# Kernel optimization log

Hardware: AMD Instinct MI355X
Metric: run time of the kernel (lower is better)

Reference implementation:

```python
import jax, jax.numpy as jnp
import numpy as np

B, H, S, D = 4, 16, 2048, 64

def setup_inputs() -> dict:
    key = jax.random.key(0)
    kq, kk, kv = jax.random.split(key, 3)
    return {
        "query": jax.random.normal(kq, (B, H, S, D), dtype=jnp.float32),
        "key": jax.random.normal(kk, (B, H, S, D), dtype=jnp.float32),
        "value": jax.random.normal(kv, (B, H, S, D), dtype=jnp.float32),
        "dropout_p": 0,
    }

def reference(query, key, value, dropout_p):
    # qk: [B,H,S,S] materialized as in the original (unfused SDPA)
    scale = query.shape[-1] ** -0.5
    qk = jnp.einsum("bhqd,bhkd->bhqk", query, key) * scale
    attn = jax.nn.softmax(qk, axis=-1)
    # dropout_p == 0 -> identity (keeps reference deterministic)
    out = jnp.einsum("bhqk,bhkd->bhqd", attn, value)
    return out
```

## Files before the change

kernel.cpp:

```cpp
#include <hip/hip_runtime.h>
#include <hip/hip_bf16.h>

#define B_   4
#define H_   16
#define SEQ  2048
#define DH   64
#define BM   128
#define BN   64
#define NBH  (B_ * H_)
#define NELEM (NBH * SEQ * DH)

typedef __bf16 bf16x8 __attribute__((ext_vector_type(8)));
typedef float  f32x4  __attribute__((ext_vector_type(4)));
typedef unsigned short u16x8 __attribute__((ext_vector_type(8)));
typedef unsigned short u16x4 __attribute__((ext_vector_type(4)));

__device__ __forceinline__ unsigned short f2bu(float x) {
    __hip_bfloat16 h = __float2bfloat16(x);
    return __builtin_bit_cast(unsigned short, h);
}

__device__ __forceinline__ void ld_lds16(const unsigned short* g, unsigned short* l) {
    __builtin_amdgcn_global_load_lds(
        (const __attribute__((address_space(1))) unsigned int*)(g),
        (__attribute__((address_space(3))) unsigned int*)(l), 16, 0, 0);
}

__global__ __launch_bounds__(256)
void prep_kv(const float* __restrict__ K, const float* __restrict__ V,
             unsigned short* __restrict__ Kb, unsigned short* __restrict__ Vt) {
    __shared__ unsigned short tile[64 * 72];
    const int bh = blockIdx.y;
    const int s0 = blockIdx.x * 64;
    const int t  = threadIdx.x;

    {
        const float* Ki = K + (size_t)bh * SEQ * DH + (size_t)s0 * DH;
        unsigned short* Ko = Kb + (size_t)bh * SEQ * DH + (size_t)s0 * DH;
        for (int jj = 0; jj < 2; ++jj) {
            const int e = (jj * 256 + t) * 8;
            const float4 a = *reinterpret_cast<const float4*>(Ki + e);
            const float4 b = *reinterpret_cast<const float4*>(Ki + e + 4);
            u16x8 u;
            u[0] = f2bu(a.x); u[1] = f2bu(a.y); u[2] = f2bu(a.z); u[3] = f2bu(a.w);
            u[4] = f2bu(b.x); u[5] = f2bu(b.y); u[6] = f2bu(b.z); u[7] = f2bu(b.w);
            *reinterpret_cast<u16x8*>(Ko + e) = u;
        }
    }

    const float* Vb = V + (size_t)bh * SEQ * DH + (size_t)s0 * DH;
    unsigned short* Vo = Vt + (size_t)bh * DH * SEQ;
    {
        const int sl = t >> 2, d0 = (t & 3) * 16;
        for (int c = 0; c < 4; ++c) {
            const float4 v = *reinterpret_cast<const float4*>(Vb + sl * DH + d0 + c * 4);
            u16x4 u; u[0] = f2bu(v.x); u[1] = f2bu(v.y); u[2] = f2bu(v.z); u[3] = f2bu(v.w);
            *reinterpret_cast<u16x4*>(&tile[sl * 72 + d0 + c * 4]) = u;
        }
    }
    __syncthreads();
    {
        const int d = t >> 2, sc0 = (t & 3) * 16;
        for (int c = 0; c < 2; ++c) {
            const int s = sc0 + c * 8;
            u16x8 u;
#pragma unroll
            for (int r = 0; r < 8; ++r) u[r] = tile[(s + r) * 72 + d];
            *reinterpret_cast<u16x8*>(Vo + (size_t)d * SEQ + s0 + s) = u;
        }
    }
}

__global__ __launch_bounds__(256, 4)
void fa_fwd(const float* __restrict__ Qg, const unsigned short* __restrict__ Kb,
            const unsigned short* __restrict__ Vtb, float* __restrict__ Og)
{
    __shared__ __attribute__((aligned(16))) unsigned short smem[16384];

    const int tid  = threadIdx.x;
    const int lane = tid & 63;
    const int wave = tid >> 6;
    const int l15  = lane & 15;
    const int quad = lane >> 4;

    const int bid   = blockIdx.x;
    const int xcd   = bid & 7;
    const int jj    = bid >> 3;
    const int bh    = (xcd << 3) | (jj >> 4);
    const int qtile = jj & 15;

    const float*          Qb  = Qg  + (size_t)bh * SEQ * DH;
    const unsigned short* Kbh = Kb  + (size_t)bh * SEQ * DH;
    const unsigned short* Vbh = Vtb + (size_t)bh * DH * SEQ;
    float*                Ob  = Og  + (size_t)bh * SEQ * DH;

    const int qrow0 = qtile * BM + wave * 32;

    const float CS = 0.125f * 1.4426950408889634f;

    bf16x8 Qf[2][2];
    for (int rt = 0; rt < 2; ++rt) {
        const float* qsrc = Qb + (size_t)(qrow0 + rt * 16 + l15) * DH + quad * 8;
        for (int kt = 0; kt < 2; ++kt) {
            const float4 a = *reinterpret_cast<const float4*>(qsrc + kt * 32);
            const float4 b = *reinterpret_cast<const float4*>(qsrc + kt * 32 + 4);
            union { bf16x8 v; unsigned short u[8]; } tmp;
            tmp.u[0] = f2bu(a.x * CS); tmp.u[1] = f2bu(a.y * CS);
            tmp.u[2] = f2bu(a.z * CS); tmp.u[3] = f2bu(a.w * CS);
            tmp.u[4] = f2bu(b.x * CS); tmp.u[5] = f2bu(b.y * CS);
            tmp.u[6] = f2bu(b.z * CS); tmp.u[7] = f2bu(b.w * CS);
            Qf[rt][kt] = tmp.v;
        }
    }

    bf16x8 ones;
    {
        union { bf16x8 v; unsigned short u[8]; } t;
        for (int i = 0; i < 8; ++i) t.u[i] = 0x3F80;
        ones = t.v;
    }
    const f32x4 fzero = {0.f, 0.f, 0.f, 0.f};

    f32x4 Oacc[2][4];
    f32x4 Lacc[2];
    for (int rt = 0; rt < 2; ++rt) {
        Lacc[rt] = fzero;
        for (int dt = 0; dt < 4; ++dt) Oacc[rt][dt] = fzero;
    }

    const unsigned short* kp[2];
    const unsigned short* vp[2];
    int koff_st[2], voff_st[2];
    for (int i = 0; i < 2; ++i) {
        const int beta = i * 256 + tid;
        {
            const int s    = beta >> 3;
            const int b    = beta & 7;
            const int gnat = b ^ (s & 7);
            const int grow = 32 * ((s >> 4) & 1) + 8 * ((s >> 2) & 3)
                           + 4 * (s >> 5) + (s & 3);
            kp[i]  = Kbh + (size_t)grow * DH + gnat * 8;
        }
        {
            const int d = beta >> 3;
            const int g = (beta & 7) ^ (d & 7);
            vp[i]  = Vbh + (size_t)d * SEQ + g * 8;
        }
        koff_st[i] = (i * 256 + wave * 64) * 8;
        voff_st[i] = 4096 + (i * 256 + wave * 64) * 8;
    }

    int krd[4][2];
#pragma unroll
    for (int nt = 0; nt < 4; ++nt) {
        const int s  = nt * 16 + l15;
        const int sx = l15 & 7;
        krd[nt][0] = s * 64 + ((quad    ) ^ sx) * 8;
        krd[nt][1] = s * 64 + ((quad + 4) ^ sx) * 8;
    }
    int vrd[2][4];
#pragma unroll
    for (int ks = 0; ks < 2; ++ks)
#pragma unroll
        for (int dt = 0; dt < 4; ++dt) {
            const int d = dt * 16 + l15;
            vrd[ks][dt] = 4096 + d * 64 + (((ks * 4 + quad) ^ (l15 & 7)) << 3);
        }

#define STAGE(BUF) do {                                                        \
        _Pragma("unroll")                                                      \
        for (int i = 0; i < 2; ++i) {                                          \
            ld_lds16(kp[i], smem + (BUF) * 8192 + koff_st[i]);                 \
            kp[i] += BN * DH;                                                  \
        }                                                                      \
        _Pragma("unroll")                                                      \
        for (int i = 0; i < 2; ++i) {                                          \
            ld_lds16(vp[i], smem + (BUF) * 8192 + voff_st[i]);                 \
            vp[i] += BN;                                                       \
        }                                                                      \
    } while (0)

#define COMPUTE(BUF) do {                                                      \
        f32x4 Sacc[2][4];                                                      \
        __builtin_amdgcn_s_setprio(1);                                         \
        _Pragma("unroll")                                                      \
        for (int nt = 0; nt < 4; ++nt) {                                       \
            const bf16x8 kf0 = *reinterpret_cast<const bf16x8*>(               \
                &smem[(BUF) * 8192 + krd[nt][0]]);                             \
            const bf16x8 kf1 = *reinterpret_cast<const bf16x8*>(               \
                &smem[(BUF) * 8192 + krd[nt][1]]);                             \
            Sacc[0][nt] = __builtin_amdgcn_mfma_f32_16x16x32_bf16(kf0, Qf[0][0], fzero,       0, 0, 0); \
            Sacc[0][nt] = __builtin_amdgcn_mfma_f32_16x16x32_bf16(kf1, Qf[0][1], Sacc[0][nt], 0, 0, 0); \
            Sacc[1][nt] = __builtin_amdgcn_mfma_f32_16x16x32_bf16(kf0, Qf[1][0], fzero,       0, 0, 0); \
            Sacc[1][nt] = __builtin_amdgcn_mfma_f32_16x16x32_bf16(kf1, Qf[1][1], Sacc[1][nt], 0, 0, 0); \
        }                                                                      \
        __builtin_amdgcn_s_setprio(0);                                         \
        bf16x8 af[2][2];                                                       \
        _Pragma("unroll")                                                      \
        for (int rt = 0; rt < 2; ++rt)                                         \
        {                                                                      \
            _Pragma("unroll")                                                  \
            for (int ks = 0; ks < 2; ++ks) {                                   \
                union { bf16x8 v; unsigned w[4]; } a;                          \
                _Pragma("unroll")                                              \
                for (int h = 0; h < 2; ++h) {                                  \
                    _Pragma("unroll")                                          \
                    for (int rp = 0; rp < 2; ++rp) {                           \
                        const float p0 = __builtin_amdgcn_exp2f(Sacc[rt][ks + 2 * h][2 * rp    ]); \
                        const float p1 = __builtin_amdgcn_exp2f(Sacc[rt][ks + 2 * h][2 * rp + 1]); \
                        const unsigned u0 = __builtin_bit_cast(unsigned, p0) + 0x8000u; \
                        const unsigned u1 = __builtin_bit_cast(unsigned, p1) + 0x8000u; \
                        a.w[h * 2 + rp] = __builtin_amdgcn_perm(u1, u0, 0x07060302u); \
                    }                                                          \
                }                                                              \
                af[rt][ks] = a.v;                                              \
                Lacc[rt] = __builtin_amdgcn_mfma_f32_16x16x32_bf16(a.v, ones, Lacc[rt], 0, 0, 0); \
            }                                                                  \
        }                                                                      \
        __builtin_amdgcn_s_setprio(1);                                         \
        _Pragma("unroll")                                                      \
        for (int ks = 0; ks < 2; ++ks) {                                       \
            _Pragma("unroll")                                                  \
            for (int dt = 0; dt < 4; ++dt) {                                   \
                const bf16x8 bfr = *reinterpret_cast<const bf16x8*>(           \
                    &smem[(BUF) * 8192 + vrd[ks][dt]]);                        \
                Oacc[0][dt] = __builtin_amdgcn_mfma_f32_16x16x32_bf16(af[0][ks], bfr, Oacc[0][dt], 0, 0, 0); \
                Oacc[1][dt] = __builtin_amdgcn_mfma_f32_16x16x32_bf16(af[1][ks], bfr, Oacc[1][dt], 0, 0, 0); \
            }                                                                  \
        }                                                                      \
        __builtin_amdgcn_s_setprio(0);                                         \
    } while (0)

    STAGE(0);
    __syncthreads();

#pragma unroll 1
    for (int it2 = 0; it2 < 15; ++it2) {
        STAGE(1);
        COMPUTE(0);
        __syncthreads();
        STAGE(0);
        COMPUTE(1);
        __syncthreads();
    }
    STAGE(1);
    COMPUTE(0);
    __syncthreads();
    COMPUTE(1);

#undef STAGE
#undef COMPUTE

    for (int rt = 0; rt < 2; ++rt) {
        for (int r = 0; r < 4; ++r) {
            const float inv = 1.0f / Lacc[rt][r];
            const int row = qrow0 + rt * 16 + quad * 4 + r;
            float* orow = Ob + (size_t)row * DH + l15;
            for (int dt = 0; dt < 4; ++dt)
                orow[dt * 16] = Oacc[rt][dt][r] * inv;
        }
    }
}

extern "C" void kernel_launch(void* const* d_in, const int* in_sizes, int n_in,
                              void* d_out, int out_size, void* d_ws, size_t ws_size,
                              hipStream_t stream) {
    const float* Q = (const float*)d_in[0];
    const float* K = (const float*)d_in[1];
    const float* V = (const float*)d_in[2];
    float* O = (float*)d_out;

    unsigned short* Kb = (unsigned short*)d_ws;
    unsigned short* Vt = Kb + (size_t)NELEM;

    prep_kv<<<dim3(SEQ / 64, NBH), 256, 0, stream>>>(K, V, Kb, Vt);
    fa_fwd<<<dim3((SEQ / BM) * NBH), dim3(256), 0, stream>>>(Q, Kb, Vt, O);
}
```

Before: 200.4 us.

## Split per-tile compute into halves to interleave QK, softmax and PV MFMAs

Changes the key-row permutation used when staging K into LDS so each half of the 64-key tile maps to one contiguous PV k-slice. The tile's compute is then split into two halves: the second QK MFMA pair is issued while the first half's exp2/pack runs, and V fragments are prefetched into registers before use. Register-resident LDS offsets shrink to a few scalars. The aim is to overlap VALU softmax work with MFMA and LDS latency, at the cost of more live registers for the bf16 V fragments.

```diff
diff --git a/kernel.cpp b/kernel.cpp
--- a/kernel.cpp
+++ b/kernel.cpp
@@ -137,8 +137,8 @@
             const int s    = beta >> 3;
             const int b    = beta & 7;
             const int gnat = b ^ (s & 7);
-            const int grow = 32 * ((s >> 4) & 1) + 8 * ((s >> 2) & 3)
-                           + 4 * (s >> 5) + (s & 3);
+            const int grow = 32 * (s >> 5) + 8 * ((s >> 2) & 3)
+                           + 4 * ((s >> 4) & 1) + (s & 3);
             kp[i]  = Kbh + (size_t)grow * DH + gnat * 8;
         }
         {
@@ -150,22 +150,11 @@
         voff_st[i] = 4096 + (i * 256 + wave * 64) * 8;
     }
 
-    int krd[4][2];
-#pragma unroll
-    for (int nt = 0; nt < 4; ++nt) {
-        const int s  = nt * 16 + l15;
-        const int sx = l15 & 7;
-        krd[nt][0] = s * 64 + ((quad    ) ^ sx) * 8;
-        krd[nt][1] = s * 64 + ((quad + 4) ^ sx) * 8;
-    }
-    int vrd[2][4];
-#pragma unroll
-    for (int ks = 0; ks < 2; ++ks)
-#pragma unroll
-        for (int dt = 0; dt < 4; ++dt) {
-            const int d = dt * 16 + l15;
-            vrd[ks][dt] = 4096 + d * 64 + (((ks * 4 + quad) ^ (l15 & 7)) << 3);
-        }
+    const int sx   = l15 & 7;
+    const int krd0 = l15 * 64 + ((quad    ) ^ sx) * 8;
+    const int krd1 = l15 * 64 + ((quad + 4) ^ sx) * 8;
+    const int vrd0 = l15 * 64 + ((quad    ) ^ sx) * 8;
+    const int vrd1 = l15 * 64 + ((quad + 4) ^ sx) * 8;
 
 #define STAGE(BUF) do {                                                        \
         _Pragma("unroll")                                                      \
@@ -180,54 +169,74 @@
         }                                                                      \
     } while (0)
 
+#define QK_PAIR(BUF, NT0, SACC) do {                                           \
+        _Pragma("unroll")                                                      \
+        for (int m = 0; m < 2; ++m) {                                          \
+            const bf16x8 kf0 = *reinterpret_cast<const bf16x8*>(               \
+                &smem[(BUF) * 8192 + ((NT0) + m) * 1024 + krd0]);              \
+            const bf16x8 kf1 = *reinterpret_cast<const bf16x8*>(               \
+                &smem[(BUF) * 8192 + ((NT0) + m) * 1024 + krd1]);              \
+            SACC[0][m] = __builtin_amdgcn_mfma_f32_16x16x32_bf16(kf0, Qf[0][0], fzero,       0, 0, 0); \
+            SACC[0][m] = __builtin_amdgcn_mfma_f32_16x16x32_bf16(kf1, Qf[0][1], SACC[0][m], 0, 0, 0); \
+            SACC[1][m] = __builtin_amdgcn_mfma_f32_16x16x32_bf16(kf0, Qf[1][0], fzero,       0, 0, 0); \
+            SACC[1][m] = __builtin_amdgcn_mfma_f32_16x16x32_bf16(kf1, Qf[1][1], SACC[1][m], 0, 0, 0); \
+        }                                                                      \
+    } while (0)
+
+#define LOAD_BFR(BUF, DST, VRD) do {                                           \
+        _Pragma("unroll")                                                      \
+        for (int dt = 0; dt < 4; ++dt)                                         \
+            DST[dt] = *reinterpret_cast<const bf16x8*>(                        \
+                &smem[(BUF) * 8192 + 4096 + dt * 1024 + (VRD)]);               \
+    } while (0)
+
+#define SM_HALF(SACC, KS) do {                                                 \
+        _Pragma("unroll")                                                      \
+        for (int rt = 0; rt < 2; ++rt) {                                       \
+            union { bf16x8 v; unsigned w[4]; } a;                              \
+            _Pragma("unroll")                                                  \
+            for (int m = 0; m < 2; ++m) {                                      \
+                _Pragma("unroll")                                              \
+                for (int rp = 0; rp < 2; ++rp) {                               \
+                    const float p0 = __builtin_amdgcn_exp2f(SACC[rt][m][2 * rp    ]); \
+                    const float p1 = __builtin_amdgcn_exp2f(SACC[rt][m][2 * rp + 1]); \
+                    const unsigned u0 = __builtin_bit_cast(unsigned, p0) + 0x8000u; \
+                    const unsigned u1 = __builtin_bit_cast(unsigned, p1) + 0x8000u; \
+                    a.w[m * 2 + rp] = __builtin_amdgcn_perm(u1, u0, 0x07060302u); \
+                }                                                              \
+            }                                                                  \
+            af[rt][KS] = a.v;                                                  \
+            Lacc[rt] = __builtin_amdgcn_mfma_f32_16x16x32_bf16(a.v, ones, Lacc[rt], 0, 0, 0); \
+        }                                                                      \
+    } while (0)
+
+#define PV_HALF(KS, BFR) do {                                                  \
+        _Pragma("unroll")                                                      \
+        for (int dt = 0; dt < 4; ++dt) {                                       \
+            Oacc[0][dt] = __builtin_amdgcn_mfma_f32_16x16x32_bf16(af[0][KS], BFR[dt], Oacc[0][dt], 0, 0, 0); \
+            Oacc[1][dt] = __builtin_amdgcn_mfma_f32_16x16x32_bf16(af[1][KS], BFR[dt], Oacc[1][dt], 0, 0, 0); \
+        }                                                                      \
+    } while (0)
+
 #define COMPUTE(BUF) do {                                                      \
-        f32x4 Sacc[2][4];                                                      \
+        f32x4 SA[2][2], SB[2][2];                                              \
+        bf16x8 bfr0[4], bfr1[4];                                               \
+        bf16x8 af[2][2];                                                       \
+                                        \
+        LOAD_BFR(BUF, bfr0, vrd0);                                             \
         __builtin_amdgcn_s_setprio(1);                                         \
-        _Pragma("unroll")                                                      \
-        for (int nt = 0; nt < 4; ++nt) {                                       \
-            const bf16x8 kf0 = *reinterpret_cast<const bf16x8*>(               \
-                &smem[(BUF) * 8192 + krd[nt][0]]);                             \
-            const bf16x8 kf1 = *reinterpret_cast<const bf16x8*>(               \
-                &smem[(BUF) * 8192 + krd[nt][1]]);                             \
-            Sacc[0][nt] = __builtin_amdgcn_mfma_f32_16x16x32_bf16(kf0, Qf[0][0], fzero,       0, 0, 0); \
-            Sacc[0][nt] = __builtin_amdgcn_mfma_f32_16x16x32_bf16(kf1, Qf[0][1], Sacc[0][nt], 0, 0, 0); \
-            Sacc[1][nt] = __builtin_amdgcn_mfma_f32_16x16x32_bf16(kf0, Qf[1][0], fzero,       0, 0, 0); \
-            Sacc[1][nt] = __builtin_amdgcn_mfma_f32_16x16x32_bf16(kf1, Qf[1][1], Sacc[1][nt], 0, 0, 0); \
-        }                                                                      \
+        QK_PAIR(BUF, 0, SA);                                                   \
         __builtin_amdgcn_s_setprio(0);                                         \
-        bf16x8 af[2][2];                                                       \
-        _Pragma("unroll")                                                      \
-        for (int rt = 0; rt < 2; ++rt)                                         \
-        {                                                                      \
-            _Pragma("unroll")                                                  \
-            for (int ks = 0; ks < 2; ++ks) {                                   \
-                union { bf16x8 v; unsigned w[4]; } a;                          \
-                _Pragma("unroll")                                              \
-                for (int h = 0; h < 2; ++h) {                                  \
-                    _Pragma("unroll")                                          \
-                    for (int rp = 0; rp < 2; ++rp) {                           \
-                        const float p0 = __builtin_amdgcn_exp2f(Sacc[rt][ks + 2 * h][2 * rp    ]); \
-                        const float p1 = __builtin_amdgcn_exp2f(Sacc[rt][ks + 2 * h][2 * rp + 1]); \
-                        const unsigned u0 = __builtin_bit_cast(unsigned, p0) + 0x8000u; \
-                        const unsigned u1 = __builtin_bit_cast(unsigned, p1) + 0x8000u; \
-                        a.w[h * 2 + rp] = __builtin_amdgcn_perm(u1, u0, 0x07060302u); \
-                    }                                                          \
-                }                                                              \
-                af[rt][ks] = a.v;                                              \
-                Lacc[rt] = __builtin_amdgcn_mfma_f32_16x16x32_bf16(a.v, ones, Lacc[rt], 0, 0, 0); \
-            }                                                                  \
-        }                                                                      \
+                                       \
+        QK_PAIR(BUF, 2, SB);                                                   \
+        SM_HALF(SA, 0);                                                        \
+                        \
+        LOAD_BFR(BUF, bfr1, vrd1);                                             \
+        SM_HALF(SB, 1);                                                        \
+        PV_HALF(0, bfr0);                                                      \
+                                             \
         __builtin_amdgcn_s_setprio(1);                                         \
-        _Pragma("unroll")                                                      \
-        for (int ks = 0; ks < 2; ++ks) {                                       \
-            _Pragma("unroll")                                                  \
-            for (int dt = 0; dt < 4; ++dt) {                                   \
-                const bf16x8 bfr = *reinterpret_cast<const bf16x8*>(           \
-                    &smem[(BUF) * 8192 + vrd[ks][dt]]);                        \
-                Oacc[0][dt] = __builtin_amdgcn_mfma_f32_16x16x32_bf16(af[0][ks], bfr, Oacc[0][dt], 0, 0, 0); \
-                Oacc[1][dt] = __builtin_amdgcn_mfma_f32_16x16x32_bf16(af[1][ks], bfr, Oacc[1][dt], 0, 0, 0); \
-            }                                                                  \
-        }                                                                      \
+        PV_HALF(1, bfr1);                                                      \
         __builtin_amdgcn_s_setprio(0);                                         \
     } while (0)
 
@@ -249,6 +258,10 @@
     COMPUTE(1);
 
 #undef STAGE
+#undef QK_PAIR
+#undef LOAD_BFR
+#undef SM_HALF
+#undef PV_HALF
 #undef COMPUTE
 
     for (int rt = 0; rt < 2; ++rt) {
```

Measured after the change: 224.8 us. 12.2% more time.

## Switch attention kernel to 32x32x16 MFMA tiles with VALU row sums

Applied to the files above, without the earlier changes.

Rewrites the QK and PV matrix products to use 32x32x16 bf16 MFMA instructions instead of 16x16x32, which changes the fragment layout, the swizzled LDS read offsets and the K staging row permutation. The softmax denominator is now accumulated with plain VALU adds plus one cross-half shuffle, replacing the extra MFMA against a ones vector. The goal is fewer MFMA issues and LDS reads per tile and removal of the extra sum MFMAs. The larger accumulators push register use up, so launch bounds drop to 3 blocks per SIMD group, which may lower occupancy.

```diff
diff --git a/kernel.cpp b/kernel.cpp
--- a/kernel.cpp
+++ b/kernel.cpp
@@ -12,6 +12,7 @@
 
 typedef __bf16 bf16x8 __attribute__((ext_vector_type(8)));
 typedef float  f32x4  __attribute__((ext_vector_type(4)));
+typedef float  f32x16 __attribute__((ext_vector_type(16)));
 typedef unsigned short u16x8 __attribute__((ext_vector_type(8)));
 typedef unsigned short u16x4 __attribute__((ext_vector_type(4)));
 
@@ -71,7 +72,7 @@
     }
 }
 
-__global__ __launch_bounds__(256, 4)
+__global__ __launch_bounds__(256, 3)
 void fa_fwd(const float* __restrict__ Qg, const unsigned short* __restrict__ Kb,
             const unsigned short* __restrict__ Vtb, float* __restrict__ Og)
 {
@@ -80,8 +81,9 @@
     const int tid  = threadIdx.x;
     const int lane = tid & 63;
     const int wave = tid >> 6;
-    const int l15  = lane & 15;
-    const int quad = lane >> 4;
+    const int l31  = lane & 31;
+    const int hi   = lane >> 5;
+    const int l7   = lane & 7;
 
     const int bid   = blockIdx.x;
     const int xcd   = bid & 7;
@@ -98,35 +100,25 @@
 
     const float CS = 0.125f * 1.4426950408889634f;
 
-    bf16x8 Qf[2][2];
-    for (int rt = 0; rt < 2; ++rt) {
-        const float* qsrc = Qb + (size_t)(qrow0 + rt * 16 + l15) * DH + quad * 8;
-        for (int kt = 0; kt < 2; ++kt) {
-            const float4 a = *reinterpret_cast<const float4*>(qsrc + kt * 32);
-            const float4 b = *reinterpret_cast<const float4*>(qsrc + kt * 32 + 4);
-            union { bf16x8 v; unsigned short u[8]; } tmp;
-            tmp.u[0] = f2bu(a.x * CS); tmp.u[1] = f2bu(a.y * CS);
-            tmp.u[2] = f2bu(a.z * CS); tmp.u[3] = f2bu(a.w * CS);
-            tmp.u[4] = f2bu(b.x * CS); tmp.u[5] = f2bu(b.y * CS);
-            tmp.u[6] = f2bu(b.z * CS); tmp.u[7] = f2bu(b.w * CS);
-            Qf[rt][kt] = tmp.v;
-        }
-    }
-
-    bf16x8 ones;
-    {
-        union { bf16x8 v; unsigned short u[8]; } t;
-        for (int i = 0; i < 8; ++i) t.u[i] = 0x3F80;
-        ones = t.v;
-    }
-    const f32x4 fzero = {0.f, 0.f, 0.f, 0.f};
-
-    f32x4 Oacc[2][4];
-    f32x4 Lacc[2];
-    for (int rt = 0; rt < 2; ++rt) {
-        Lacc[rt] = fzero;
-        for (int dt = 0; dt < 4; ++dt) Oacc[rt][dt] = fzero;
-    }
+    bf16x8 Qf[4];
+#pragma unroll
+    for (int kt = 0; kt < 4; ++kt) {
+        const float* qsrc = Qb + (size_t)(qrow0 + l31) * DH + kt * 16 + hi * 8;
+        const float4 a = *reinterpret_cast<const float4*>(qsrc);
+        const float4 b = *reinterpret_cast<const float4*>(qsrc + 4);
+        union { bf16x8 v; unsigned short u[8]; } tmp;
+        tmp.u[0] = f2bu(a.x * CS); tmp.u[1] = f2bu(a.y * CS);
+        tmp.u[2] = f2bu(a.z * CS); tmp.u[3] = f2bu(a.w * CS);
+        tmp.u[4] = f2bu(b.x * CS); tmp.u[5] = f2bu(b.y * CS);
+        tmp.u[6] = f2bu(b.z * CS); tmp.u[7] = f2bu(b.w * CS);
+        Qf[kt] = tmp.v;
+    }
+
+    const f32x16 z16 = {0.f,0.f,0.f,0.f, 0.f,0.f,0.f,0.f,
+                        0.f,0.f,0.f,0.f, 0.f,0.f,0.f,0.f};
+
+    f32x16 OA = z16, OB = z16;
+    float Lp0 = 0.f, Lp1 = 0.f;
 
     const unsigned short* kp[2];
     const unsigned short* vp[2];
@@ -137,8 +129,8 @@
             const int s    = beta >> 3;
             const int b    = beta & 7;
             const int gnat = b ^ (s & 7);
-            const int grow = 32 * ((s >> 4) & 1) + 8 * ((s >> 2) & 3)
-                           + 4 * (s >> 5) + (s & 3);
+            const int grow = (s & 3) + 4 * ((s >> 3) & 1) + 8 * ((s >> 2) & 1)
+                           + 16 * ((s >> 4) & 1) + 32 * (s >> 5);
             kp[i]  = Kbh + (size_t)grow * DH + gnat * 8;
         }
         {
@@ -150,22 +142,10 @@
         voff_st[i] = 4096 + (i * 256 + wave * 64) * 8;
     }
 
-    int krd[4][2];
-#pragma unroll
-    for (int nt = 0; nt < 4; ++nt) {
-        const int s  = nt * 16 + l15;
-        const int sx = l15 & 7;
-        krd[nt][0] = s * 64 + ((quad    ) ^ sx) * 8;
-        krd[nt][1] = s * 64 + ((quad + 4) ^ sx) * 8;
-    }
-    int vrd[2][4];
-#pragma unroll
-    for (int ks = 0; ks < 2; ++ks)
-#pragma unroll
-        for (int dt = 0; dt < 4; ++dt) {
-            const int d = dt * 16 + l15;
-            vrd[ks][dt] = 4096 + d * 64 + (((ks * 4 + quad) ^ (l15 & 7)) << 3);
-        }
+    int rdoff[4];
+#pragma unroll
+    for (int c = 0; c < 4; ++c)
+        rdoff[c] = l31 * 64 + ((((c << 1) | hi) ^ l7) << 3);
 
 #define STAGE(BUF) do {                                                        \
         _Pragma("unroll")                                                      \
@@ -180,54 +160,62 @@
         }                                                                      \
     } while (0)
 
+#define QK_TILE(BUF, T, S) do {                                                \
+        _Pragma("unroll")                                                      \
+        for (int kt = 0; kt < 4; ++kt) {                                       \
+            const bf16x8 kf = *reinterpret_cast<const bf16x8*>(                \
+                &smem[(BUF) * 8192 + (T) * 2048 + rdoff[kt]]);                 \
+            S = __builtin_amdgcn_mfma_f32_32x32x16_bf16(kf, Qf[kt],            \
+                    (kt == 0) ? z16 : S, 0, 0, 0);                             \
+        }                                                                      \
+    } while (0)
+
+#define SM_TILE(S, T) do {                                                     \
+        float p[16];                                                           \
+        _Pragma("unroll")                                                      \
+        for (int r = 0; r < 16; ++r) p[r] = __builtin_amdgcn_exp2f(S[r]);      \
+        _Pragma("unroll")                                                      \
+        for (int c1 = 0; c1 < 2; ++c1) {                                       \
+            union { bf16x8 v; unsigned w[4]; } a;                              \
+            _Pragma("unroll")                                                  \
+            for (int w = 0; w < 4; ++w) {                                      \
+                const unsigned u0 = __builtin_bit_cast(unsigned, p[8*c1 + 2*w    ]) + 0x8000u; \
+                const unsigned u1 = __builtin_bit_cast(unsigned, p[8*c1 + 2*w + 1]) + 0x8000u; \
+                a.w[w] = __builtin_amdgcn_perm(u1, u0, 0x07060302u);           \
+            }                                                                  \
+            af[2 * (T) + c1] = a.v;                                            \
+        }                                                                      \
+        _Pragma("unroll")                                                      \
+        for (int r = 0; r < 8; ++r)  Lp0 += p[r];                              \
+        _Pragma("unroll")                                                      \
+        for (int r = 8; r < 16; ++r) Lp1 += p[r];                              \
+    } while (0)
+
+#define PV_ALL(BUF) do {                                                       \
+        _Pragma("unroll")                                                      \
+        for (int m = 0; m < 4; ++m) {                                          \
+            const bf16x8 bv0 = *reinterpret_cast<const bf16x8*>(               \
+                &smem[(BUF) * 8192 + 4096 + rdoff[m]]);                        \
+            const bf16x8 bv1 = *reinterpret_cast<const bf16x8*>(               \
+                &smem[(BUF) * 8192 + 4096 + 2048 + rdoff[m]]);                 \
+            OA = __builtin_amdgcn_mfma_f32_32x32x16_bf16(af[m], bv0, OA, 0, 0, 0); \
+            OB = __builtin_amdgcn_mfma_f32_32x32x16_bf16(af[m], bv1, OB, 0, 0, 0); \
+        }                                                                      \
+    } while (0)
+
 #define COMPUTE(BUF) do {                                                      \
-        f32x4 Sacc[2][4];                                                      \
+        bf16x8 af[4];                                                          \
+        f32x16 S;                                                              \
         __builtin_amdgcn_s_setprio(1);                                         \
-        _Pragma("unroll")                                                      \
-        for (int nt = 0; nt < 4; ++nt) {                                       \
-            const bf16x8 kf0 = *reinterpret_cast<const bf16x8*>(               \
-                &smem[(BUF) * 8192 + krd[nt][0]]);                             \
-            const bf16x8 kf1 = *reinterpret_cast<const bf16x8*>(               \
-                &smem[(BUF) * 8192 + krd[nt][1]]);                             \
-            Sacc[0][nt] = __builtin_amdgcn_mfma_f32_16x16x32_bf16(kf0, Qf[0][0], fzero,       0, 0, 0); \
-            Sacc[0][nt] = __builtin_amdgcn_mfma_f32_16x16x32_bf16(kf1, Qf[0][1], Sacc[0][nt], 0, 0, 0); \
-            Sacc[1][nt] = __builtin_amdgcn_mfma_f32_16x16x32_bf16(kf0, Qf[1][0], fzero,       0, 0, 0); \
-            Sacc[1][nt] = __builtin_amdgcn_mfma_f32_16x16x32_bf16(kf1, Qf[1][1], Sacc[1][nt], 0, 0, 0); \
-        }                                                                      \
+        QK_TILE(BUF, 0, S);                                                    \
         __builtin_amdgcn_s_setprio(0);                                         \
-        bf16x8 af[2][2];                                                       \
-        _Pragma("unroll")                                                      \
-        for (int rt = 0; rt < 2; ++rt)                                         \
-        {                                                                      \
-            _Pragma("unroll")                                                  \
-            for (int ks = 0; ks < 2; ++ks) {                                   \
-                union { bf16x8 v; unsigned w[4]; } a;                          \
-                _Pragma("unroll")                                              \
-                for (int h = 0; h < 2; ++h) {                                  \
-                    _Pragma("unroll")                                          \
-                    for (int rp = 0; rp < 2; ++rp) {                           \
-                        const float p0 = __builtin_amdgcn_exp2f(Sacc[rt][ks + 2 * h][2 * rp    ]); \
-                        const float p1 = __builtin_amdgcn_exp2f(Sacc[rt][ks + 2 * h][2 * rp + 1]); \
-                        const unsigned u0 = __builtin_bit_cast(unsigned, p0) + 0x8000u; \
-                        const unsigned u1 = __builtin_bit_cast(unsigned, p1) + 0x8000u; \
-                        a.w[h * 2 + rp] = __builtin_amdgcn_perm(u1, u0, 0x07060302u); \
-                    }                                                          \
-                }                                                              \
-                af[rt][ks] = a.v;                                              \
-                Lacc[rt] = __builtin_amdgcn_mfma_f32_16x16x32_bf16(a.v, ones, Lacc[rt], 0, 0, 0); \
-            }                                                                  \
-        }                                                                      \
+        SM_TILE(S, 0);                                                         \
         __builtin_amdgcn_s_setprio(1);                                         \
-        _Pragma("unroll")                                                      \
-        for (int ks = 0; ks < 2; ++ks) {                                       \
-            _Pragma("unroll")                                                  \
-            for (int dt = 0; dt < 4; ++dt) {                                   \
-                const bf16x8 bfr = *reinterpret_cast<const bf16x8*>(           \
-                    &smem[(BUF) * 8192 + vrd[ks][dt]]);                        \
-                Oacc[0][dt] = __builtin_amdgcn_mfma_f32_16x16x32_bf16(af[0][ks], bfr, Oacc[0][dt], 0, 0, 0); \
-                Oacc[1][dt] = __builtin_amdgcn_mfma_f32_16x16x32_bf16(af[1][ks], bfr, Oacc[1][dt], 0, 0, 0); \
-            }                                                                  \
-        }                                                                      \
+        QK_TILE(BUF, 1, S);                                                    \
+        __builtin_amdgcn_s_setprio(0);                                         \
+        SM_TILE(S, 1);                                                         \
+        __builtin_amdgcn_s_setprio(1);                                         \
+        PV_ALL(BUF);                                                           \
         __builtin_amdgcn_s_setprio(0);                                         \
     } while (0)
 
@@ -249,16 +237,26 @@
     COMPUTE(1);
 
 #undef STAGE
+#undef QK_TILE
+#undef SM_TILE
+#undef PV_ALL
 #undef COMPUTE
 
-    for (int rt = 0; rt < 2; ++rt) {
-        for (int r = 0; r < 4; ++r) {
-            const float inv = 1.0f / Lacc[rt][r];
-            const int row = qrow0 + rt * 16 + quad * 4 + r;
-            float* orow = Ob + (size_t)row * DH + l15;
-            for (int dt = 0; dt < 4; ++dt)
-                orow[dt * 16] = Oacc[rt][dt][r] * inv;
-        }
+    float Lsum = Lp0 + Lp1;
+    Lsum += __shfl_xor(Lsum, 32, 64);
+    const float invq = 1.0f / Lsum;
+    const int hi16 = hi << 4;
+
+#pragma unroll
+    for (int r = 0; r < 16; ++r) {
+        const int qb = (r & 3) + 8 * (r >> 2);
+        const float invr = __builtin_bit_cast(float,
+            __builtin_amdgcn_ds_bpermute((qb << 2) + hi16,
+                                         __builtin_bit_cast(int, invq)));
+        const int row = qrow0 + qb + 4 * hi;
+        float* orow = Ob + (size_t)row * DH + l31;
+        orow[0]  = OA[r] * invr;
+        orow[32] = OB[r] * invr;
     }
 }
 
```

Measured after the change: 206.0 us. 1.03x slower.
